# Kernel optimization log

Hardware: AMD Instinct MI355X
Metric: run time of the kernel (lower is better)

The kernel has to match this reference:

```python
import jax, jax.numpy as jnp
import numpy as np

HEADS = 4
NBLK = 4
UPS = 4
EPS = 1e-5


def conv3x3(x, w, b):
    # x: NCHW, w: OIHW (3x3, stride 1, pad 1 -> SAME)
    y = jax.lax.conv_general_dilated(x, w, (1, 1), 'SAME',
                                     dimension_numbers=('NCHW', 'OIHW', 'NCHW'))
    return y + b[None, :, None, None]


def layer_norm(x, g, b):
    mu = jnp.mean(x, axis=-1, keepdims=True)
    var = jnp.var(x, axis=-1, keepdims=True)
    return (x - mu) * jax.lax.rsqrt(var + EPS) * g + b


def attention(x, wq, bq, wp, bp):
    # NOTE: the torch module's reshape flattens all windows into one sequence,
    # so this is mathematically global attention over all H*W tokens.
    B, H, W, C = x.shape
    L = H * W
    hd = C // HEADS
    t = x.reshape(B, L, C)
    qkv = (t @ wq + bq).reshape(B, L, 3, HEADS, hd).transpose(2, 0, 3, 1, 4)
    q, k, v = qkv[0], qkv[1], qkv[2]                      # (B, nh, L, hd)
    attn = jax.nn.softmax(jnp.einsum('bnld,bnmd->bnlm', q, k) * (hd ** -0.5), axis=-1)
    o = jnp.einsum('bnlm,bnmd->bnld', attn, v)            # (B, nh, L, hd)
    o = o.transpose(0, 2, 1, 3).reshape(B, L, C)
    return (o @ wp + bp).reshape(B, H, W, C)


def swin_block(x, g1, b1, wq, bq, wp, bp, g2, b2, w1, bf1, w2, bf2):
    shortcut = x
    h = jnp.transpose(x, (0, 2, 3, 1))                    # NHWC
    h = layer_norm(h, g1, b1)
    h = attention(h, wq, bq, wp, bp) + h
    h = layer_norm(h, g2, b2)
    h = (jax.nn.gelu(h @ w1 + bf1, approximate=False) @ w2 + bf2) + h
    return shortcut + jnp.transpose(h, (0, 3, 1, 2))


def pixel_shuffle(x, r):
    B, C, H, W = x.shape
    c = C // (r * r)
    x = x.reshape(B, c, r, r, H, W).transpose(0, 1, 4, 2, 5, 3)
    return x.reshape(B, c, H * r, W * r)


def setup_inputs() -> dict:
    key = jax.random.key(0)
    ks = jax.random.split(key, 16)
    d = 48

    def rn(k, shape, s=0.02):
        return jax.random.normal(k, shape, jnp.float32) * s

    return {
        'x': jax.random.normal(ks[0], (2, 3, 64, 64), jnp.float32),
        'conv_first_w': rn(ks[1], (d, 3, 3, 3)),
        'conv_first_b': jnp.zeros((d,), jnp.float32),
        'norm1_g': jnp.ones((NBLK, d), jnp.float32),
        'norm1_b': jnp.zeros((NBLK, d), jnp.float32),
        'qkv_w': rn(ks[2], (NBLK, d, 3 * d)),
        'qkv_b': jnp.zeros((NBLK, 3 * d), jnp.float32),
        'proj_w': rn(ks[3], (NBLK, d, d)),
        'proj_b': jnp.zeros((NBLK, d), jnp.float32),
        'norm2_g': jnp.ones((NBLK, d), jnp.float32),
        'norm2_b': jnp.zeros((NBLK, d), jnp.float32),
        'fc1_w': rn(ks[4], (NBLK, d, 2 * d)),
        'fc1_b': jnp.zeros((NBLK, 2 * d), jnp.float32),
        'fc2_w': rn(ks[5], (NBLK, 2 * d, d)),
        'fc2_b': jnp.zeros((NBLK, d), jnp.float32),
        'up_w': rn(ks[6], (d * UPS * UPS, d, 3, 3)),
        'up_b': jnp.zeros((d * UPS * UPS,), jnp.float32),
        'last_w': rn(ks[7], (3, d, 3, 3)),
        'last_b': jnp.zeros((3,), jnp.float32),
    }


def reference(x, conv_first_w, conv_first_b, norm1_g, norm1_b, qkv_w, qkv_b,
              proj_w, proj_b, norm2_g, norm2_b, fc1_w, fc1_b, fc2_w, fc2_b,
              up_w, up_b, last_w, last_b):
    h = conv3x3(x, conv_first_w, conv_first_b)
    for i in range(NBLK):
        h = swin_block(h, norm1_g[i], norm1_b[i], qkv_w[i], qkv_b[i],
                       proj_w[i], proj_b[i], norm2_g[i], norm2_b[i],
                       fc1_w[i], fc1_b[i], fc2_w[i], fc2_b[i])
    h = conv3x3(h, up_w, up_b)
    h = pixel_shuffle(h, UPS)
    return conv3x3(h, last_w, last_b)
```

## Files before the change

kernel.cpp:

```cpp
#include <hip/hip_runtime.h>
#include <hip/hip_bf16.h>
#include <math.h>

#define BB 2
#define D 48
#define HH 64
#define WW 64
#define LL 4096
#define NHEADS 4
#define HD 12
#define NBLK 4
#define CUP 768
#define H2 256
#define W2 256

#define NSPLIT 4
#define OPART_STRIDE 393216

typedef __attribute__((ext_vector_type(8))) short short8v;
typedef __attribute__((ext_vector_type(4))) float f32x4;
typedef unsigned long long u64;

__device__ __forceinline__ short f2bf(float f) {
    __hip_bfloat16 h = __float2bfloat16(f);
    union { __hip_bfloat16 b; short s; } u; u.b = h; return u.s;
}
__device__ __forceinline__ float bf2f(short s) {
    union { float f; unsigned u; } x;
    x.u = ((unsigned)(unsigned short)s) << 16;
    return x.f;
}
__device__ __forceinline__ float exp2_raw(float x) {
    float r; asm("v_exp_f32 %0, %1" : "=v"(r) : "v"(x)); return r;
}

__global__ void conv3x3_kernel(const float* __restrict__ in, const float* __restrict__ w,
                               const float* __restrict__ bias, float* __restrict__ out,
                               int Cin, int Cout) {
    int idx = blockIdx.x * blockDim.x + threadIdx.x;
    int total = BB * Cout * HH * WW;
    if (idx >= total) return;
    int x = idx % WW;
    int y = (idx / WW) % HH;
    int co = (idx / (WW * HH)) % Cout;
    int b = idx / (WW * HH * Cout);
    float s = bias[co];
    for (int ci = 0; ci < Cin; ci++) {
        const float* ip = in + ((size_t)(b * Cin + ci) * HH) * WW;
        const float* wp = w + (size_t)(co * Cin + ci) * 9;
        #pragma unroll
        for (int ky = 0; ky < 3; ky++) {
            int iy = y + ky - 1;
            if (iy < 0 || iy >= HH) continue;
            #pragma unroll
            for (int kx = 0; kx < 3; kx++) {
                int ix = x + kx - 1;
                if (ix < 0 || ix >= WW) continue;
                s += ip[iy * WW + ix] * wp[ky * 3 + kx];
            }
        }
    }
    out[idx] = s;
}

__global__ __launch_bounds__(256) void pack_h_kernel(const float* __restrict__ h,
                                                     short* __restrict__ hbfp) {
    int idx = blockIdx.x * 256 + threadIdx.x;
    const int TOT = 2 * 66 * 66 * 48;
    if (idx >= TOT + 64) return;
    if (idx >= TOT) { hbfp[idx] = 0; return; }
    int ci = idx % 48;
    int p = idx / 48;
    int xx = p % 66;
    int q = p / 66;
    int yy = q % 66;
    int b = q / 66;
    short v = 0;
    if (yy >= 1 && yy <= 64 && xx >= 1 && xx <= 64)
        v = f2bf(h[((size_t)(b * 48 + ci) << 12) + (yy - 1) * 64 + (xx - 1)]);
    hbfp[idx] = v;
}

__global__ __launch_bounds__(256) void pack_w_kernel(const float* __restrict__ w,
                                                     short* __restrict__ Wp) {
    int idx = blockIdx.x * 256 + threadIdx.x;
    if (idx >= 48 * 14 * 512) return;
    int j = idx & 7;
    int g = (idx >> 3) & 3;
    int col = (idx >> 5) & 15;
    int s = (idx >> 9) % 14;
    int n16 = idx / (14 * 512);
    int k = 32 * s + 8 * g + j;
    short v = 0;
    if (k < 432) {
        int tap = k / 48, ci = k - tap * 48;
        int co = n16 * 16 + col;
        v = f2bf(w[((size_t)co * 48 + ci) * 9 + tap]);
    }
    Wp[idx] = v;
}

__global__ __launch_bounds__(256) void pack_lw_kernel(const float* __restrict__ w,
                                                      short* __restrict__ Wp2) {
    int idx = blockIdx.x * 256 + threadIdx.x;
    if (idx >= 14 * 512) return;
    int j = idx & 7;
    int g = (idx >> 3) & 3;
    int col = (idx >> 5) & 15;
    int s = idx >> 9;
    int k = 32 * s + 8 * g + j;
    short v = 0;
    if (k < 432 && col < 3) {
        int tap = k / 48, ci = k - tap * 48;
        v = f2bf(w[((size_t)col * 48 + ci) * 9 + tap]);
    }
    Wp2[idx] = v;
}

#define CU_LOADB(P, n) { \
    _Pragma("unroll") \
    for (int s_ = 0; s_ < 14; s_++) \
        P[s_] = *(const short8v*)(Wb + (size_t)(n) * 7168 + s_ * 512); }

#define CU_COMP(P, n) { \
    f32x4 acc = {0.f, 0.f, 0.f, 0.f}; \
    _Pragma("unroll") \
    for (int s_ = 0; s_ < 14; s_++) \
        acc = __builtin_amdgcn_mfma_f32_16x16x32_bf16(av[s_], P[s_], acc, 0, 0, 0); \
    float bval = bias[(n) * 16 + col]; \
    _Pragma("unroll") \
    for (int j = 0; j < 4; j++) \
        Sw[sbase + j * 192 + (n)] = f2bf(acc[j] + bval); }

__global__ __launch_bounds__(128) void conv_up_mfma_kernel(const short* __restrict__ hbfp,
                                                           const short* __restrict__ Wp,
                                                           const float* __restrict__ bias,
                                                           short* __restrict__ U) {
    __shared__ short Sb[2][12288];
    int tid = threadIdx.x;
    int wave = tid >> 6, lane = tid & 63;
    int mt = blockIdx.x * 2 + wave;
    int b = mt >> 8;
    int rem = mt & 255;
    int y = rem >> 2;
    int xt = rem & 3;
    int col = lane & 15;
    int g = lane >> 4;
    int x = xt * 16 + col;

    const short* zb = hbfp + 2 * 66 * 66 * 48;

    short8v av[14];
    #pragma unroll
    for (int s = 0; s < 14; s++) {
        int gg = 4 * s + g;
        int tap = (gg * 171) >> 10;
        int cig = gg - tap * 6;
        int dy = (tap * 11) >> 5;
        int dx = tap - dy * 3;
        const short* ap = hbfp + ((size_t)((b * 66 + y + dy) * 66 + (x + dx)) * 48 + cig * 8);
        ap = (gg < 54) ? ap : zb;
        av[s] = *(const short8v*)ap;
    }

    const short* Wb = Wp + col * 32 + g * 8;
    short* Sw = Sb[wave];
    int dyq = col >> 2, dxq = col & 3;
    int sbase = dyq * 3072 + (16 * g + dxq) * 48;

    short8v Ba[14], Bb[14];
    CU_LOADB(Ba, 0);
    for (int n = 0; n < 48; n += 2) {
        CU_LOADB(Bb, n + 1);
        CU_COMP(Ba, n);
        if (n + 2 < 48) CU_LOADB(Ba, n + 2);
        CU_COMP(Bb, n + 1);
    }

    short* Ub = U + (((size_t)(b * 256 + 4 * y) * 256) + xt * 64) * 48;
    for (int i = lane; i < 1536; i += 64) {
        int row = i / 384;
        int w8 = i - row * 384;
        short8v v = *(const short8v*)(Sw + (size_t)i * 8);
        *(short8v*)(Ub + (size_t)row * 256 * 48 + w8 * 8) = v;
    }
}

__global__ void zero16_kernel(u64* __restrict__ p, int n) {
    int i = blockIdx.x * 256 + threadIdx.x;
    if (i >= n) return;
    u64 fill = 0ull;
    int rel = 8 * i - 2097152;
    if (rel >= 0 && rel < 524288 && (((rel >> 5) & 15) == 12))
        fill = 0x3F803F803F803F80ull;
    p[2 * i] = fill;
    p[2 * i + 1] = fill;
}

__global__ __launch_bounds__(256) void fused_ln1_qkv_kernel(
    const float* __restrict__ hsrc, const float* __restrict__ g1, const float* __restrict__ b1,
    const float* __restrict__ w, const float* __restrict__ bias,
    float* __restrict__ ln1, short* __restrict__ Qbf, short* __restrict__ Kbf,
    short* __restrict__ Vr) {
    __shared__ float hs[48 * 17];
    __shared__ float lnr[16 * 49];
    __shared__ float wl[48 * 144];
    int blk = blockIdx.x;
    int b = blk >> 8;
    int pos0 = (blk & 255) * 16;
    int tid = threadIdx.x;

    for (int i = tid; i < 48 * 144; i += 256) wl[i] = w[i];
    for (int i = tid; i < 48 * 16; i += 256) {
        int ch = i >> 4, p = i & 15;
        hs[ch * 17 + p] = hsrc[((size_t)b * 48 + ch) * 4096 + pos0 + p];
    }
    __syncthreads();

    int tok = tid >> 4, oct = tid & 15;
    int pos = pos0 + tok;
    float v[3];
    float s = 0.f, s2 = 0.f;
    #pragma unroll
    for (int j = 0; j < 3; j++) {
        float x = hs[(oct * 3 + j) * 17 + tok];
        v[j] = x; s += x; s2 += x * x;
    }
    #pragma unroll
    for (int msk = 1; msk < 16; msk <<= 1) {
        s += __shfl_xor(s, msk, 64);
        s2 += __shfl_xor(s2, msk, 64);
    }
    float mu = s * (1.f / 48.f);
    float var = s2 * (1.f / 48.f) - mu * mu;
    float rs = rsqrtf(var + 1e-5f);
    float* go = ln1 + ((size_t)b * 4096 + pos) * 48 + oct * 3;
    #pragma unroll
    for (int j = 0; j < 3; j++) {
        int c = oct * 3 + j;
        float y = (v[j] - mu) * rs * g1[c] + b1[c];
        lnr[tok * 49 + c] = y;
        go[j] = y;
    }
    __syncthreads();

    int c0 = oct * 9;
    float acc[9];
    #pragma unroll
    for (int j = 0; j < 9; j++) acc[j] = bias[c0 + j];
    #pragma unroll 4
    for (int k = 0; k < 48; k++) {
        float a = lnr[tok * 49 + k];
        const float* wr = wl + k * 144 + c0;
        #pragma unroll
        for (int j = 0; j < 9; j++) acc[j] += a * wr[j];
    }

    const float scale = 0.41647023f;
    int sstep = pos >> 5, r = pos & 31;
    int g2 = (r < 16) ? (r >> 2) : ((r - 16) >> 2);
    int j2 = (r < 16) ? (r & 3) : 4 + ((r - 16) & 3);
    #pragma unroll
    for (int j = 0; j < 9; j++) {
        int c = c0 + j;
        int which = (c >= 96) ? 2 : (c >= 48 ? 1 : 0);
        int rem = c - which * 48;
        int hh = rem / 12;
        int dd = rem - hh * 12;
        int bh = b * 4 + hh;
        if (which == 0)
            Qbf[((size_t)bh * 4096 + pos) * 32 + dd] = f2bf(acc[j] * scale);
        else if (which == 1)
            Kbf[((size_t)bh * 4096 + pos) * 32 + dd] = f2bf(acc[j]);
        else
            Vr[((size_t)bh * 128 + sstep) * 512 + dd * 32 + g2 * 8 + j2] = f2bf(acc[j]);
    }
}

__global__ __launch_bounds__(256) void fused_mlp_kernel(
    const float* __restrict__ opart, const float* __restrict__ ssump,
    const float* __restrict__ pwg, const float* __restrict__ pb,
    const float* __restrict__ ln1, const float* __restrict__ g2v, const float* __restrict__ b2v,
    const float* __restrict__ f1w, const float* __restrict__ f1b,
    const float* __restrict__ f2w, const float* __restrict__ f2b,
    float* __restrict__ hbuf) {
    __shared__ float sm[14640];
    float* wp  = sm;
    float* w1  = sm + 2304;
    float* w2  = sm + 6912;
    float* arf = sm + 11520;
    float* lnr = sm + 12304;
    float* m1v = sm + 13088;

    int blk = blockIdx.x;
    int b = blk >> 8;
    int pos0 = (blk & 255) * 16;
    int tid = threadIdx.x;

    for (int i = tid; i < 2304; i += 256) wp[i] = pwg[i];
    for (int i = tid; i < 4608; i += 256) w1[i] = f1w[i];
    for (int i = tid; i < 4608; i += 256) w2[i] = f2w[i];
    for (int i = tid; i < 768; i += 256) {
        int t = i / 48, c = i - (i / 48) * 48;
        int hh = c / 12;
        size_t base = ((size_t)b * 4096 + pos0) * 48 + i;
        float stot = 0.f, s = 0.f;
        #pragma unroll
        for (int sp = 0; sp < NSPLIT; sp++) {
            stot += ssump[((size_t)sp * 8 + b * 4 + hh) * 4096 + pos0 + t];
            s += opart[base + (size_t)sp * OPART_STRIDE];
        }
        arf[t * 49 + c] = s / stot;
    }
    __syncthreads();

    int tok = tid >> 4, oct = tid & 15;
    size_t gtok = (size_t)b * 4096 + pos0 + tok;
    int c0 = oct * 3;
    float acc[3];
    #pragma unroll
    for (int j = 0; j < 3; j++) acc[j] = pb[c0 + j];
    #pragma unroll 4
    for (int k = 0; k < 48; k++) {
        float a = arf[tok * 49 + k];
        const float* wr = wp + k * 48 + c0;
        #pragma unroll
        for (int j = 0; j < 3; j++) acc[j] += a * wr[j];
    }
    const float* rp = ln1 + gtok * 48 + c0;
    float x[3]; float s = 0.f, s2 = 0.f;
    #pragma unroll
    for (int j = 0; j < 3; j++) {
        float t = acc[j] + rp[j];
        x[j] = t; s += t; s2 += t * t;
    }
    #pragma unroll
    for (int msk = 1; msk < 16; msk <<= 1) {
        s += __shfl_xor(s, msk, 64);
        s2 += __shfl_xor(s2, msk, 64);
    }
    float mu = s * (1.f / 48.f), var = s2 * (1.f / 48.f) - mu * mu;
    float rs = rsqrtf(var + 1e-5f);
    #pragma unroll
    for (int j = 0; j < 3; j++) {
        int c = c0 + j;
        lnr[tok * 49 + c] = (x[j] - mu) * rs * g2v[c] + b2v[c];
    }
    __syncthreads();

    int d0 = oct * 6;
    float a2[6];
    #pragma unroll
    for (int j = 0; j < 6; j++) a2[j] = f1b[d0 + j];
    #pragma unroll 4
    for (int k = 0; k < 48; k++) {
        float a = lnr[tok * 49 + k];
        const float* wr = w1 + k * 96 + d0;
        #pragma unroll
        for (int j = 0; j < 6; j++) a2[j] += a * wr[j];
    }
    #pragma unroll
    for (int j = 0; j < 6; j++) {
        float g = a2[j];
        m1v[tok * 97 + d0 + j] = 0.5f * g * (1.f + erff(g * 0.70710678118654752f));
    }
    __syncthreads();

    float f2acc[3];
    #pragma unroll
    for (int j = 0; j < 3; j++) f2acc[j] = f2b[c0 + j];
    #pragma unroll 4
    for (int k = 0; k < 96; k++) {
        float a = m1v[tok * 97 + k];
        const float* wr = w2 + k * 48 + c0;
        #pragma unroll
        for (int j = 0; j < 3; j++) f2acc[j] += a * wr[j];
    }
    __syncthreads();
    #pragma unroll
    for (int j = 0; j < 3; j++)
        arf[tok * 49 + c0 + j] = f2acc[j] + lnr[tok * 49 + c0 + j];
    __syncthreads();

    for (int i = tid; i < 768; i += 256) {
        int c = i >> 4, t = i & 15;
        hbuf[(((size_t)(b * 48 + c)) << 12) + pos0 + t] += arf[t * 49 + c];
    }
}

#define LOADCH(P, c) { \
    _Pragma("unroll") \
    for (int s_ = 0; s_ < 4; s_++) { \
        const short* kp_ = Kb + ((size_t)((c) * 128 + s_ * 32 + col)) * 32 + g * 8; \
        P##k0[s_] = *(const short8v*)(kp_); \
        P##k1[s_] = *(const short8v*)(kp_ + 512); \
        P##v[s_]  = *(const short8v*)(Vrb + ((c) * 4 + s_) * 512 + vbase); \
    } }

#define STEP2(kc0, kc1, vv) { \
    f32x4 z_ = {0.f, 0.f, 0.f, 0.f}; \
    f32x4 sa1 = __builtin_amdgcn_mfma_f32_16x16x32_bf16(kc0, qb0, z_, 0, 0, 0); \
    f32x4 sa2 = __builtin_amdgcn_mfma_f32_16x16x32_bf16(kc1, qb0, z_, 0, 0, 0); \
    f32x4 sb1 = __builtin_amdgcn_mfma_f32_16x16x32_bf16(kc0, qb1, z_, 0, 0, 0); \
    f32x4 sb2 = __builtin_amdgcn_mfma_f32_16x16x32_bf16(kc1, qb1, z_, 0, 0, 0); \
    float a0 = exp2_raw(sa1[0]), a1 = exp2_raw(sa1[1]); \
    float a2 = exp2_raw(sa1[2]), a3 = exp2_raw(sa1[3]); \
    float a4 = exp2_raw(sa2[0]), a5 = exp2_raw(sa2[1]); \
    float a6 = exp2_raw(sa2[2]), a7 = exp2_raw(sa2[3]); \
    float e0 = exp2_raw(sb1[0]), e1 = exp2_raw(sb1[1]); \
    float e2 = exp2_raw(sb1[2]), e3 = exp2_raw(sb1[3]); \
    float e4 = exp2_raw(sb2[0]), e5 = exp2_raw(sb2[1]); \
    float e6 = exp2_raw(sb2[2]), e7 = exp2_raw(sb2[3]); \
    union { short8v sv; unsigned u[4]; } pa_, pe_; \
    asm("v_cvt_pk_bf16_f32 %0, %1, %2" : "=v"(pa_.u[0]) : "v"(a0), "v"(a1)); \
    asm("v_cvt_pk_bf16_f32 %0, %1, %2" : "=v"(pa_.u[1]) : "v"(a2), "v"(a3)); \
    asm("v_cvt_pk_bf16_f32 %0, %1, %2" : "=v"(pa_.u[2]) : "v"(a4), "v"(a5)); \
    asm("v_cvt_pk_bf16_f32 %0, %1, %2" : "=v"(pa_.u[3]) : "v"(a6), "v"(a7)); \
    asm("v_cvt_pk_bf16_f32 %0, %1, %2" : "=v"(pe_.u[0]) : "v"(e0), "v"(e1)); \
    asm("v_cvt_pk_bf16_f32 %0, %1, %2" : "=v"(pe_.u[1]) : "v"(e2), "v"(e3)); \
    asm("v_cvt_pk_bf16_f32 %0, %1, %2" : "=v"(pe_.u[2]) : "v"(e4), "v"(e5)); \
    asm("v_cvt_pk_bf16_f32 %0, %1, %2" : "=v"(pe_.u[3]) : "v"(e6), "v"(e7)); \
    o0 = __builtin_amdgcn_mfma_f32_16x16x32_bf16(vv, pa_.sv, o0, 0, 0, 0); \
    o1 = __builtin_amdgcn_mfma_f32_16x16x32_bf16(vv, pe_.sv, o1, 0, 0, 0); }

#define COMPUTECH2(P) { \
    STEP2(P##k0[0], P##k1[0], P##v[0]); \
    STEP2(P##k0[1], P##k1[1], P##v[1]); \
    STEP2(P##k0[2], P##k1[2], P##v[2]); \
    STEP2(P##k0[3], P##k1[3], P##v[3]); }

__global__ __launch_bounds__(256) void attn_mfma_kernel(const short* __restrict__ Qbf,
                                                        const short* __restrict__ Kbf,
                                                        const short* __restrict__ Vr,
                                                        float* __restrict__ opart,
                                                        float* __restrict__ ssump) {
    int bid = blockIdx.x;
    int bh = bid & 7;
    int qblk = (bid >> 3) & 31;
    int split = bid >> 8;
    int h = bh & 3, b = bh >> 2;
    int tid = threadIdx.x;
    int wave = tid >> 6;
    int lane = tid & 63;
    int q0 = qblk * 128 + wave * 32;
    int col = lane & 15;
    int g = lane >> 4;

    const short* Kb  = Kbf + (size_t)bh * LL * 32 + (size_t)split * 1024 * 32;
    const short* Vrb = Vr + (size_t)bh * 65536 + (size_t)split * 32 * 512;
    int vbase = col * 32 + g * 8;

    short8v qb0 = *(const short8v*)(Qbf + ((size_t)bh * LL + q0 + col) * 32 + g * 8);
    short8v qb1 = *(const short8v*)(Qbf + ((size_t)bh * LL + q0 + 16 + col) * 32 + g * 8);

    f32x4 o0 = {0.f, 0.f, 0.f, 0.f};
    f32x4 o1 = {0.f, 0.f, 0.f, 0.f};

    short8v a_k0[4], a_k1[4], a_v[4];
    short8v b_k0[4], b_k1[4], b_v[4];

    LOADCH(a_, 0);
    for (int c = 0; c < 8; c += 2) {
        LOADCH(b_, c + 1);
        COMPUTECH2(a_);
        if (c + 2 < 8) LOADCH(a_, c + 2);
        COMPUTECH2(b_);
    }

    float ssa = __shfl(o0[0], 48 + col, 64);
    float ssb = __shfl(o1[0], 48 + col, 64);

    float* op = opart + (size_t)split * OPART_STRIDE
              + ((size_t)b * 4096 + q0 + col) * 48 + h * HD;
    #pragma unroll
    for (int j = 0; j < 4; j++) {
        int d = 4 * g + j;
        if (d < HD) {
            op[d] = o0[j];
            op[16 * 48 + d] = o1[j];
        }
    }
    if (lane < 16) {
        float* sp = ssump + ((size_t)split * 8 + bh) * 4096 + q0 + col;
        sp[0] = ssa;
        sp[16] = ssb;
    }
}

__global__ __launch_bounds__(256) void lastconv_mfma_kernel(const short* __restrict__ U,
                                                            const short* __restrict__ Wp2,
                                                            const short* __restrict__ zb,
                                                            const float* __restrict__ bias,
                                                            float* __restrict__ out) {
    int tid = threadIdx.x;
    int wave = tid >> 6, lane = tid & 63;
    int t = blockIdx.x * 4 + wave;
    int xt = t & 15;
    int yy = (t >> 4) & 255;
    int b = t >> 12;
    int col = lane & 15, g = lane >> 4;
    int x = xt * 16 + col;

    const short* Ub = U + (size_t)b * 65536 * 48;
    const short* Bp = Wp2 + col * 32 + g * 8;

    f32x4 acc = {0.f, 0.f, 0.f, 0.f};
    #pragma unroll
    for (int s = 0; s < 14; s++) {
        int gg = 4 * s + g;
        int tap = (gg * 171) >> 10;
        int cig = gg - tap * 6;
        int dy3 = (tap * 11) >> 5;
        int dy = dy3 - 1;
        int dx = tap - dy3 * 3 - 1;
        int yq = yy + dy, xq = x + dx;
        bool ok = (gg < 54) && (yq >= 0) && (yq < 256) && (xq >= 0) && (xq < 256);
        const short* ap = Ub + (ptrdiff_t)(yq * 256 + xq) * 48 + cig * 8;
        ap = ok ? ap : zb;
        short8v av = *(const short8v*)ap;
        short8v bv = *(const short8v*)(Bp + s * 512);
        acc = __builtin_amdgcn_mfma_f32_16x16x32_bf16(av, bv, acc, 0, 0, 0);
    }

    if (col < 3) {
        float bval = bias[col];
        float* op = out + ((size_t)(b * 3 + col) * 256 + yy) * 256 + xt * 16 + 4 * g;
        #pragma unroll
        for (int j = 0; j < 4; j++)
            op[j] = acc[j] + bval;
    }
}

static inline int gs(int n) { return (n + 255) / 256; }

extern "C" void kernel_launch(void* const* d_in, const int* in_sizes, int n_in,
                              void* d_out, int out_size, void* d_ws, size_t ws_size,
                              hipStream_t stream) {
    const float* x    = (const float*)d_in[0];
    const float* cf_w = (const float*)d_in[1];
    const float* cf_b = (const float*)d_in[2];
    const float* n1g  = (const float*)d_in[3];
    const float* n1b  = (const float*)d_in[4];
    const float* qkvw = (const float*)d_in[5];
    const float* qkvb = (const float*)d_in[6];
    const float* pw   = (const float*)d_in[7];
    const float* pb   = (const float*)d_in[8];
    const float* n2g  = (const float*)d_in[9];
    const float* n2b  = (const float*)d_in[10];
    const float* f1w  = (const float*)d_in[11];
    const float* f1b  = (const float*)d_in[12];
    const float* f2w  = (const float*)d_in[13];
    const float* f2b  = (const float*)d_in[14];
    const float* upw  = (const float*)d_in[15];
    const float* upb  = (const float*)d_in[16];
    const float* lw   = (const float*)d_in[17];
    const float* lb   = (const float*)d_in[18];

    float* ws = (float*)d_ws;
    const int S_h = BB * D * LL;
    float* A_h   = ws;
    float* pool  = ws + S_h;
    float* A_ln1 = pool;

    short* U_bf = (short*)pool;
    float* o_part = pool + 1572864;
    short* Qbf  = (short*)(pool + 3538944);
    short* Kbf  = Qbf + BB * NHEADS * LL * 32;
    short* Vr   = Kbf + BB * NHEADS * LL * 32;
    short* hbfp = (short*)(pool + 4849664);
    short* Wp   = (short*)(pool + 5058784);
    short* Wp2  = (short*)(pool + 5230816);
    float* ssum_part = pool + 5898240;

    conv3x3_kernel<<<gs(S_h), 256, 0, stream>>>(x, cf_w, cf_b, A_h, 3, D);

    zero16_kernel<<<1536, 256, 0, stream>>>((u64*)Qbf, 393216);
    pack_w_kernel<<<1344, 256, 0, stream>>>(upw, Wp);
    pack_lw_kernel<<<28, 256, 0, stream>>>(lw, Wp2);

    for (int i = 0; i < NBLK; i++) {
        fused_ln1_qkv_kernel<<<512, 256, 0, stream>>>(
            A_h, n1g + i * D, n1b + i * D,
            qkvw + (size_t)i * D * 3 * D, qkvb + i * 3 * D,
            A_ln1, Qbf, Kbf, Vr);
        attn_mfma_kernel<<<8 * 32 * NSPLIT, 256, 0, stream>>>(Qbf, Kbf, Vr, o_part, ssum_part);
        fused_mlp_kernel<<<512, 256, 0, stream>>>(
            o_part, ssum_part, pw + (size_t)i * D * D, pb + i * D,
            A_ln1, n2g + i * D, n2b + i * D,
            f1w + (size_t)i * D * 2 * D, f1b + i * 2 * D,
            f2w + (size_t)i * 2 * D * D, f2b + i * D,
            A_h);
    }

    pack_h_kernel<<<1634, 256, 0, stream>>>(A_h, hbfp);
    conv_up_mfma_kernel<<<256, 128, 0, stream>>>(hbfp, Wp, upb, U_bf);

    lastconv_mfma_kernel<<<2048, 256, 0, stream>>>(
        U_bf, Wp2, hbfp + 2 * 66 * 66 * 48, lb, (float*)d_out);
}
```

Baseline: 293.1 us.

## Process 64 queries per wave in attention to reuse K/V fragments

Each wave in the attention kernel now handles four 16-query fragments instead of two, so every loaded K/V chunk feeds twice as many MFMAs. The grid shrinks from 1024 to 512 blocks, with the indexing and output writes adjusted to match. This halves global K/V load traffic per query. In exchange it uses more accumulator and Q registers and launches fewer blocks, which may reduce occupancy and latency hiding on the 256-CU device.

```diff
diff --git a/kernel.cpp b/kernel.cpp
--- a/kernel.cpp
+++ b/kernel.cpp
@@ -397,37 +397,29 @@
         P##v[s_]  = *(const short8v*)(Vrb + ((c) * 4 + s_) * 512 + vbase); \
     } }
 
-#define STEP2(kc0, kc1, vv) { \
-    f32x4 z_ = {0.f, 0.f, 0.f, 0.f}; \
-    f32x4 sa1 = __builtin_amdgcn_mfma_f32_16x16x32_bf16(kc0, qb0, z_, 0, 0, 0); \
-    f32x4 sa2 = __builtin_amdgcn_mfma_f32_16x16x32_bf16(kc1, qb0, z_, 0, 0, 0); \
-    f32x4 sb1 = __builtin_amdgcn_mfma_f32_16x16x32_bf16(kc0, qb1, z_, 0, 0, 0); \
-    f32x4 sb2 = __builtin_amdgcn_mfma_f32_16x16x32_bf16(kc1, qb1, z_, 0, 0, 0); \
-    float a0 = exp2_raw(sa1[0]), a1 = exp2_raw(sa1[1]); \
-    float a2 = exp2_raw(sa1[2]), a3 = exp2_raw(sa1[3]); \
-    float a4 = exp2_raw(sa2[0]), a5 = exp2_raw(sa2[1]); \
-    float a6 = exp2_raw(sa2[2]), a7 = exp2_raw(sa2[3]); \
-    float e0 = exp2_raw(sb1[0]), e1 = exp2_raw(sb1[1]); \
-    float e2 = exp2_raw(sb1[2]), e3 = exp2_raw(sb1[3]); \
-    float e4 = exp2_raw(sb2[0]), e5 = exp2_raw(sb2[1]); \
-    float e6 = exp2_raw(sb2[2]), e7 = exp2_raw(sb2[3]); \
-    union { short8v sv; unsigned u[4]; } pa_, pe_; \
-    asm("v_cvt_pk_bf16_f32 %0, %1, %2" : "=v"(pa_.u[0]) : "v"(a0), "v"(a1)); \
-    asm("v_cvt_pk_bf16_f32 %0, %1, %2" : "=v"(pa_.u[1]) : "v"(a2), "v"(a3)); \
-    asm("v_cvt_pk_bf16_f32 %0, %1, %2" : "=v"(pa_.u[2]) : "v"(a4), "v"(a5)); \
-    asm("v_cvt_pk_bf16_f32 %0, %1, %2" : "=v"(pa_.u[3]) : "v"(a6), "v"(a7)); \
-    asm("v_cvt_pk_bf16_f32 %0, %1, %2" : "=v"(pe_.u[0]) : "v"(e0), "v"(e1)); \
-    asm("v_cvt_pk_bf16_f32 %0, %1, %2" : "=v"(pe_.u[1]) : "v"(e2), "v"(e3)); \
-    asm("v_cvt_pk_bf16_f32 %0, %1, %2" : "=v"(pe_.u[2]) : "v"(e4), "v"(e5)); \
-    asm("v_cvt_pk_bf16_f32 %0, %1, %2" : "=v"(pe_.u[3]) : "v"(e6), "v"(e7)); \
-    o0 = __builtin_amdgcn_mfma_f32_16x16x32_bf16(vv, pa_.sv, o0, 0, 0, 0); \
-    o1 = __builtin_amdgcn_mfma_f32_16x16x32_bf16(vv, pe_.sv, o1, 0, 0, 0); }
-
-#define COMPUTECH2(P) { \
-    STEP2(P##k0[0], P##k1[0], P##v[0]); \
-    STEP2(P##k0[1], P##k1[1], P##v[1]); \
-    STEP2(P##k0[2], P##k1[2], P##v[2]); \
-    STEP2(P##k0[3], P##k1[3], P##v[3]); }
+#define STEP4(kc0, kc1, vv) { \
+    _Pragma("unroll") \
+    for (int f_ = 0; f_ < 4; f_++) { \
+        f32x4 z_ = {0.f, 0.f, 0.f, 0.f}; \
+        f32x4 s1 = __builtin_amdgcn_mfma_f32_16x16x32_bf16(kc0, qb[f_], z_, 0, 0, 0); \
+        f32x4 s2 = __builtin_amdgcn_mfma_f32_16x16x32_bf16(kc1, qb[f_], z_, 0, 0, 0); \
+        float p0 = exp2_raw(s1[0]), p1 = exp2_raw(s1[1]); \
+        float p2 = exp2_raw(s1[2]), p3 = exp2_raw(s1[3]); \
+        float p4 = exp2_raw(s2[0]), p5 = exp2_raw(s2[1]); \
+        float p6 = exp2_raw(s2[2]), p7 = exp2_raw(s2[3]); \
+        union { short8v sv; unsigned u[4]; } pu_; \
+        asm("v_cvt_pk_bf16_f32 %0, %1, %2" : "=v"(pu_.u[0]) : "v"(p0), "v"(p1)); \
+        asm("v_cvt_pk_bf16_f32 %0, %1, %2" : "=v"(pu_.u[1]) : "v"(p2), "v"(p3)); \
+        asm("v_cvt_pk_bf16_f32 %0, %1, %2" : "=v"(pu_.u[2]) : "v"(p4), "v"(p5)); \
+        asm("v_cvt_pk_bf16_f32 %0, %1, %2" : "=v"(pu_.u[3]) : "v"(p6), "v"(p7)); \
+        o[f_] = __builtin_amdgcn_mfma_f32_16x16x32_bf16(vv, pu_.sv, o[f_], 0, 0, 0); \
+    } }
+
+#define COMPUTECH4(P) { \
+    STEP4(P##k0[0], P##k1[0], P##v[0]); \
+    STEP4(P##k0[1], P##k1[1], P##v[1]); \
+    STEP4(P##k0[2], P##k1[2], P##v[2]); \
+    STEP4(P##k0[3], P##k1[3], P##v[3]); }
 
 __global__ __launch_bounds__(256) void attn_mfma_kernel(const short* __restrict__ Qbf,
                                                         const short* __restrict__ Kbf,
@@ -436,13 +428,13 @@
                                                         float* __restrict__ ssump) {
     int bid = blockIdx.x;
     int bh = bid & 7;
-    int qblk = (bid >> 3) & 31;
-    int split = bid >> 8;
+    int qblk = (bid >> 3) & 15;
+    int split = bid >> 7;
     int h = bh & 3, b = bh >> 2;
     int tid = threadIdx.x;
     int wave = tid >> 6;
     int lane = tid & 63;
-    int q0 = qblk * 128 + wave * 32;
+    int q0 = qblk * 256 + wave * 64;
     int col = lane & 15;
     int g = lane >> 4;
 
@@ -450,11 +442,13 @@
     const short* Vrb = Vr + (size_t)bh * 65536 + (size_t)split * 32 * 512;
     int vbase = col * 32 + g * 8;
 
-    short8v qb0 = *(const short8v*)(Qbf + ((size_t)bh * LL + q0 + col) * 32 + g * 8);
-    short8v qb1 = *(const short8v*)(Qbf + ((size_t)bh * LL + q0 + 16 + col) * 32 + g * 8);
-
-    f32x4 o0 = {0.f, 0.f, 0.f, 0.f};
-    f32x4 o1 = {0.f, 0.f, 0.f, 0.f};
+    short8v qb[4];
+    f32x4 o[4];
+    #pragma unroll
+    for (int f = 0; f < 4; f++) {
+        qb[f] = *(const short8v*)(Qbf + ((size_t)bh * LL + q0 + 16 * f + col) * 32 + g * 8);
+        o[f] = (f32x4){0.f, 0.f, 0.f, 0.f};
+    }
 
     short8v a_k0[4], a_k1[4], a_v[4];
     short8v b_k0[4], b_k1[4], b_v[4];
@@ -462,28 +456,24 @@
     LOADCH(a_, 0);
     for (int c = 0; c < 8; c += 2) {
         LOADCH(b_, c + 1);
-        COMPUTECH2(a_);
+        COMPUTECH4(a_);
         if (c + 2 < 8) LOADCH(a_, c + 2);
-        COMPUTECH2(b_);
-    }
-
-    float ssa = __shfl(o0[0], 48 + col, 64);
-    float ssb = __shfl(o1[0], 48 + col, 64);
-
-    float* op = opart + (size_t)split * OPART_STRIDE
-              + ((size_t)b * 4096 + q0 + col) * 48 + h * HD;
-    #pragma unroll
-    for (int j = 0; j < 4; j++) {
-        int d = 4 * g + j;
-        if (d < HD) {
-            op[d] = o0[j];
-            op[16 * 48 + d] = o1[j];
+        COMPUTECH4(b_);
+    }
+
+    #pragma unroll
+    for (int f = 0; f < 4; f++) {
+        float ss = __shfl(o[f][0], 48 + col, 64);
+        float* op = opart + (size_t)split * OPART_STRIDE
+                  + ((size_t)b * 4096 + q0 + 16 * f + col) * 48 + h * HD;
+        #pragma unroll
+        for (int j = 0; j < 4; j++) {
+            int d = 4 * g + j;
+            if (d < HD)
+                op[d] = o[f][j];
         }
-    }
-    if (lane < 16) {
-        float* sp = ssump + ((size_t)split * 8 + bh) * 4096 + q0 + col;
-        sp[0] = ssa;
-        sp[16] = ssb;
+        if (lane < 16)
+            ssump[((size_t)split * 8 + bh) * 4096 + q0 + 16 * f + col] = ss;
     }
 }
 
@@ -583,7 +573,7 @@
             A_h, n1g + i * D, n1b + i * D,
             qkvw + (size_t)i * D * 3 * D, qkvb + i * 3 * D,
             A_ln1, Qbf, Kbf, Vr);
-        attn_mfma_kernel<<<8 * 32 * NSPLIT, 256, 0, stream>>>(Qbf, Kbf, Vr, o_part, ssum_part);
+        attn_mfma_kernel<<<8 * 16 * NSPLIT, 256, 0, stream>>>(Qbf, Kbf, Vr, o_part, ssum_part);
         fused_mlp_kernel<<<512, 256, 0, stream>>>(
             o_part, ssum_part, pw + (size_t)i * D * D, pb + i * D,
             A_ln1, n2g + i * D, n2b + i * D,
```

New measurement: 278.9 us. 1.05x faster.
